# Performance work log

Measured on AMD Instinct MI355X. Metric: run time of the kernel, lower is better.

## Reference

```python
import jax, jax.numpy as jnp
import numpy as np

NEG_SLOPE = 0.2  # PyG GATConv default leaky_relu negative_slope
BN_EPS = 1e-5


def gat_layer(x, src, dst, W, a_src, a_dst, bias):
    """PyG-style GATConv (self-loops already appended to src/dst).
    x: [N, F_in], W: [F_in, H*C], a_src/a_dst: [H, C], bias: [H*C].
    Returns [N, H*C] (concat heads)."""
    N = x.shape[0]
    H, C = a_src.shape
    h = (x @ W).reshape(N, H, C)                      # [N, H, C]
    al_src = jnp.sum(h * a_src[None], axis=-1)        # [N, H]
    al_dst = jnp.sum(h * a_dst[None], axis=-1)        # [N, H]
    e = jax.nn.leaky_relu(al_src[src] + al_dst[dst], NEG_SLOPE)  # [E, H]
    # segment softmax over destination neighborhoods
    m = jax.ops.segment_max(e, dst, num_segments=N)   # [N, H]
    ee = jnp.exp(e - m[dst])
    denom = jax.ops.segment_sum(ee, dst, num_segments=N)  # [N, H]
    alpha = ee / denom[dst]                           # [E, H]
    out = jax.ops.segment_sum(alpha[:, :, None] * h[src], dst, num_segments=N)  # [N, H, C]
    return out.reshape(N, H * C) + bias


def batch_norm(x, gamma, beta):
    mu = jnp.mean(x, axis=0)
    var = jnp.var(x, axis=0)  # biased, matches torch BN training stats
    return gamma * (x - mu) * jax.lax.rsqrt(var + BN_EPS) + beta


def setup_inputs() -> dict:
    key = jax.random.key(0)
    N, F, H, C = 50000, 128, 4, 64
    E = 400000
    HC = H * C  # 256
    ks = jax.random.split(key, 24)

    def glorot(k, shape, fan_in):
        return jax.random.normal(k, shape, dtype=jnp.float32) * (1.0 / np.sqrt(fan_in))

    inp = {
        "x": jax.random.normal(ks[0], (N, F), dtype=jnp.float32),
        "edge_index": jax.random.randint(ks[1], (2, E), 0, N, dtype=jnp.int64),
        # conv1: F -> H*C
        "W1": glorot(ks[2], (F, HC), F),
        "a1s": glorot(ks[3], (H, C), C),
        "a1d": glorot(ks[4], (H, C), C),
        "b1": jnp.zeros((HC,), jnp.float32),
        # conv2: H*C -> H*C
        "W2": glorot(ks[5], (HC, HC), HC),
        "a2s": glorot(ks[6], (H, C), C),
        "a2d": glorot(ks[7], (H, C), C),
        "b2": jnp.zeros((HC,), jnp.float32),
        # conv3: H*C -> C (1 head)
        "W3": glorot(ks[8], (HC, C), HC),
        "a3s": glorot(ks[9], (1, C), C),
        "a3d": glorot(ks[10], (1, C), C),
        "b3": jnp.zeros((C,), jnp.float32),
        # batch norms
        "g1": jnp.ones((HC,), jnp.float32),
        "be1": jnp.zeros((HC,), jnp.float32),
        "g2": jnp.ones((HC,), jnp.float32),
        "be2": jnp.zeros((HC,), jnp.float32),
        # MLP head: C -> C//2 -> 2
        "fw1": glorot(ks[11], (C, C // 2), C),
        "fb1": jnp.zeros((C // 2,), jnp.float32),
        "fw2": glorot(ks[12], (C // 2, 2), C // 2),
        "fb2": jnp.zeros((2,), jnp.float32),
    }
    return inp


def reference(x, edge_index, W1, a1s, a1d, b1, W2, a2s, a2d, b2,
              W3, a3s, a3d, b3, g1, be1, g2, be2, fw1, fb1, fw2, fb2):
    N = x.shape[0]
    loop = jnp.arange(N, dtype=edge_index.dtype)
    src = jnp.concatenate([edge_index[0], loop])  # self-loops (PyG default)
    dst = jnp.concatenate([edge_index[1], loop])

    h = gat_layer(x, src, dst, W1, a1s, a1d, b1)
    h = jax.nn.elu(batch_norm(h, g1, be1))
    h = gat_layer(h, src, dst, W2, a2s, a2d, b2)
    h = jax.nn.elu(batch_norm(h, g2, be2))
    h = jax.nn.elu(gat_layer(h, src, dst, W3, a3s, a3d, b3))
    h = jax.nn.relu(h @ fw1 + fb1)
    return h @ fw2 + fb2  # [N, 2] logits
```

## Files before the change

### kernel.cpp

```cpp
#include <hip/hip_runtime.h>
#include <math.h>
#include <stdint.h>

typedef __attribute__((ext_vector_type(8))) short short8v;
typedef __attribute__((ext_vector_type(4))) float float4v;

__device__ __forceinline__ float bf2f(unsigned short u) {
  return __uint_as_float((unsigned int)u << 16);
}
__device__ __forceinline__ unsigned short f2bf(float f) {
  unsigned int u = __float_as_uint(f);
  unsigned int r = (u + 0x7FFFu + ((u >> 16) & 1u)) >> 16;
  return (unsigned short)r;
}
__device__ __forceinline__ float exp_lrelu(float x) {
  x = x > 0.f ? x : 0.2f * x;
  return expf(x);
}

__device__ __forceinline__ void wprep_one(const float* W, unsigned short* Wh,
                                          int t, int K, int Nw)
{
  int i = t & 7;
  int lane = (t >> 3) & 63;
  int frag = t >> 9;
  int ktiles = K >> 5;
  int n_tile = frag / ktiles, k_tile = frag - n_tile * ktiles;
  int k = k_tile * 32 + ((lane >> 4) << 3) + i;
  int n = (n_tile << 4) + (lane & 15);
  Wh[t] = f2bf(W[(size_t)k * Nw + n]);
}

__global__ void wprep_all_kernel(const float* __restrict__ W1, unsigned short* __restrict__ w1h,
                                 const float* __restrict__ W2, unsigned short* __restrict__ w2h,
                                 const float* __restrict__ W3, unsigned short* __restrict__ w3h)
{
  int t = blockIdx.x * 256 + threadIdx.x;
  const int s1 = 128 * 256, s2 = 256 * 256, s3 = 256 * 64;
  if (t < s1) { wprep_one(W1, w1h, t, 128, 256); return; }
  t -= s1;
  if (t < s2) { wprep_one(W2, w2h, t, 256, 256); return; }
  t -= s2;
  if (t < s3) { wprep_one(W3, w3h, t, 256, 64); }
}

template<int MI, int WM, int WN, int KSTEPS, int HEADS, bool SRCF32>
__global__ __launch_bounds__(128) void gemm_bn_al(
    const void* __restrict__ AsrcV,
    const float* __restrict__ scale, const float* __restrict__ shift,
    const unsigned short* __restrict__ Bh,
    const float* __restrict__ a_s, const float* __restrict__ a_d,
    unsigned short* __restrict__ C, float* __restrict__ al_s, float* __restrict__ al_d,
    int M)
{
  constexpr int BM = WM * MI * 16;
  constexpr int Nw = HEADS * 64;
  constexpr int K = KSTEPS * 64;
  constexpr int KT32 = KSTEPS * 2;
  __shared__ __align__(16) unsigned char smem[2][8192];

  const int tid = threadIdx.x;
  const int wid = tid >> 6, lane = tid & 63;
  const int wm = wid / WN, wn = wid % WN;
  const int gn = blockIdx.y * WN + wn;
  const int m0 = blockIdx.x * BM;
  const int n0 = gn * 64;
  const int ar = lane & 15;
  const int cchunk = lane >> 4;
  const int ntile0 = n0 >> 4;
  const int srow = min(m0 + (tid & 63), M - 1);

  float4v acc[MI][4];
#pragma unroll
  for (int mi = 0; mi < MI; ++mi)
#pragma unroll
    for (int ni = 0; ni < 4; ++ni)
      acc[mi][ni] = (float4v){0.f, 0.f, 0.f, 0.f};

  float4 rv0[4], rv1[4];
  short8v ru[4];

  auto LOADS = [&](int ks) {
#pragma unroll
    for (int j = 0; j < 4; ++j) {
      int c = 2 * j + wid;
      if constexpr (SRCF32) {
        const float* p = (const float*)AsrcV + (size_t)srow * K + ks * 64 + c * 8;
        rv0[j] = *(const float4*)p;
        rv1[j] = *(const float4*)(p + 4);
      } else {
        const unsigned short* p = (const unsigned short*)AsrcV + (size_t)srow * K + ks * 64 + c * 8;
        ru[j] = *(const short8v*)p;
      }
    }
  };
  auto XWRITE = [&](int buf, int ks) {
#pragma unroll
    for (int j = 0; j < 4; ++j) {
      int c = 2 * j + wid;
      int r = tid & 63;
      short8v wv;
      if constexpr (SRCF32) {
        float v[8] = {rv0[j].x, rv0[j].y, rv0[j].z, rv0[j].w,
                      rv1[j].x, rv1[j].y, rv1[j].z, rv1[j].w};
#pragma unroll
        for (int i = 0; i < 8; ++i) wv[i] = (short)f2bf(v[i]);
      } else {
        int f = ks * 64 + c * 8;
        float4 sc0 = *(const float4*)(scale + f), sc1 = *(const float4*)(scale + f + 4);
        float4 sh0 = *(const float4*)(shift + f), sh1 = *(const float4*)(shift + f + 4);
        float sc[8] = {sc0.x, sc0.y, sc0.z, sc0.w, sc1.x, sc1.y, sc1.z, sc1.w};
        float sh[8] = {sh0.x, sh0.y, sh0.z, sh0.w, sh1.x, sh1.y, sh1.z, sh1.w};
#pragma unroll
        for (int i = 0; i < 8; ++i) {
          float t = fmaf(bf2f((unsigned short)ru[j][i]), sc[i], sh[i]);
          t = t > 0.f ? t : expm1f(t);
          wv[i] = (short)f2bf(t);
        }
      }
      *(short8v*)&smem[buf][c * 1024 + r * 16] = wv;
    }
  };

  LOADS(0);
  XWRITE(0, 0);
  int cur = 0;
  for (int ks = 0; ks < KSTEPS; ++ks) {
    __syncthreads();
    short8v bh[2][4];
#pragma unroll
    for (int hh = 0; hh < 2; ++hh)
#pragma unroll
      for (int ni = 0; ni < 4; ++ni) {
        int kt = ks * 2 + hh;
        size_t off = (((size_t)(ntile0 + ni) * KT32 + kt) * 64 + lane) * 8;
        bh[hh][ni] = *(const short8v*)(Bh + off);
      }
    if (ks + 1 < KSTEPS) LOADS(ks + 1);
    short8v ah[2][MI];
#pragma unroll
    for (int hh = 0; hh < 2; ++hh)
#pragma unroll
      for (int mi = 0; mi < MI; ++mi) {
        int row = wm * MI * 16 + mi * 16 + ar;
        int c = hh * 4 + cchunk;
        ah[hh][mi] = *(const short8v*)&smem[cur][c * 1024 + row * 16];
      }
#pragma unroll
    for (int hh = 0; hh < 2; ++hh)
#pragma unroll
      for (int mi = 0; mi < MI; ++mi)
#pragma unroll
        for (int ni = 0; ni < 4; ++ni)
          acc[mi][ni] = __builtin_amdgcn_mfma_f32_16x16x32_bf16(ah[hh][mi], bh[hh][ni], acc[mi][ni], 0, 0, 0);
    if (ks + 1 < KSTEPS) XWRITE(cur ^ 1, ks + 1);
    cur ^= 1;
  }

  const int cc = lane & 15;
#pragma unroll
  for (int mi = 0; mi < MI; ++mi) {
    int rowb = m0 + wm * MI * 16 + mi * 16 + ((lane >> 4) << 2);
#pragma unroll
    for (int r = 0; r < 4; ++r) {
      int row = rowb + r;
      if (row < M) {
#pragma unroll
        for (int ni = 0; ni < 4; ++ni)
          C[(size_t)row * Nw + n0 + ni * 16 + cc] = f2bf(acc[mi][ni][r]);
      }
    }
  }

  const int head = (HEADS == 4) ? gn : 0;
  float as_[4], ad_[4];
#pragma unroll
  for (int ni = 0; ni < 4; ++ni) {
    as_[ni] = a_s[head * 64 + ni * 16 + cc];
    ad_[ni] = a_d[head * 64 + ni * 16 + cc];
  }
#pragma unroll
  for (int mi = 0; mi < MI; ++mi) {
#pragma unroll
    for (int r = 0; r < 4; ++r) {
      float h0 = bf2f(f2bf(acc[mi][0][r]));
      float h1 = bf2f(f2bf(acc[mi][1][r]));
      float h2 = bf2f(f2bf(acc[mi][2][r]));
      float h3 = bf2f(f2bf(acc[mi][3][r]));
      float ps = h0 * as_[0] + h1 * as_[1] + h2 * as_[2] + h3 * as_[3];
      float pd = h0 * ad_[0] + h1 * ad_[1] + h2 * ad_[2] + h3 * ad_[3];
#pragma unroll
      for (int off = 1; off < 16; off <<= 1) {
        ps += __shfl_xor(ps, off);
        pd += __shfl_xor(pd, off);
      }
      int row = m0 + wm * MI * 16 + mi * 16 + ((lane >> 4) << 2) + r;
      if (cc == 0 && row < M) {
        al_s[row * HEADS + head] = ps;
        al_d[row * HEADS + head] = pd;
      }
    }
  }
}

__global__ void count_kernel(const int* __restrict__ dst, int E, int Etot, int* __restrict__ counts)
{
  int e = blockIdx.x * 256 + threadIdx.x;
  if (e >= Etot) return;
  int d = (e < E) ? dst[e] : (e - E);
  atomicAdd(&counts[d], 1);
}

__global__ void block_sum_kernel(const int* __restrict__ counts, int N, int* __restrict__ bsums)
{
  __shared__ int sd[256];
  int i = blockIdx.x * 256 + threadIdx.x;
  sd[threadIdx.x] = (i < N) ? counts[i] : 0;
  __syncthreads();
  for (int off = 128; off; off >>= 1) {
    if (threadIdx.x < off) sd[threadIdx.x] += sd[threadIdx.x + off];
    __syncthreads();
  }
  if (threadIdx.x == 0) bsums[blockIdx.x] = sd[0];
}

__global__ void scan_bsums_kernel(int* bsums, int nb)
{
  __shared__ int sd[256];
  int t = threadIdx.x;
  int v = (t < nb) ? bsums[t] : 0;
  sd[t] = v;
  __syncthreads();
  for (int off = 1; off < 256; off <<= 1) {
    int x = (t >= off) ? sd[t - off] : 0;
    __syncthreads();
    sd[t] += x;
    __syncthreads();
  }
  if (t < nb) bsums[t] = sd[t] - v;
}

__global__ void scan_write_kernel(const int* __restrict__ counts, int N,
                                  const int* __restrict__ bsums, int* __restrict__ rowStart, int Etot)
{
  __shared__ int sd[256];
  int i = blockIdx.x * 256 + threadIdx.x;
  int v = (i < N) ? counts[i] : 0;
  sd[threadIdx.x] = v;
  __syncthreads();
  for (int off = 1; off < 256; off <<= 1) {
    int x = (threadIdx.x >= off) ? sd[threadIdx.x - off] : 0;
    __syncthreads();
    sd[threadIdx.x] += x;
    __syncthreads();
  }
  if (i < N) rowStart[i] = bsums[blockIdx.x] + sd[threadIdx.x] - v;
  if (i == N - 1) rowStart[N] = Etot;
}

__global__ void fill_kernel(const int* __restrict__ src, const int* __restrict__ dst,
                            int E, int Etot, const int* __restrict__ rowStart,
                            int* __restrict__ cursor, int* __restrict__ csrSrc)
{
  int e = blockIdx.x * 256 + threadIdx.x;
  if (e >= Etot) return;
  int s, d;
  if (e < E) { s = src[e]; d = dst[e]; } else { s = d = e - E; }
  int pos = rowStart[d] + atomicAdd(&cursor[d], 1);
  csrSrc[pos] = s;
}

__global__ __launch_bounds__(256) void aggregate_fused4(
    const unsigned short* __restrict__ h16,
    const float* __restrict__ als, const float* __restrict__ ald,
    const int* __restrict__ csrSrc, const int* __restrict__ rowStart,
    unsigned short* __restrict__ outp, int N)
{
  __shared__ float ldsW[4][256];
  const int wl = threadIdx.x >> 6;
  int wid = blockIdx.x * 4 + wl;
  if (wid >= N) return;
  const int lane = threadIdx.x & 63;
  const int head = lane >> 4;
  const int start = rowStart[wid], end = rowStart[wid + 1];

  float4 adv = ((const float4*)ald)[wid];
  float acc[4] = {};
  float wsum = 0.f;

  for (int base = start; base < end; base += 64) {
    int cnt = end - base; if (cnt > 64) cnt = 64;
    int s_l = 0;
    if (lane < cnt) {
      s_l = csrSrc[base + lane];
      float4 av = ((const float4*)als)[s_l];
      float4 w4;
      w4.x = exp_lrelu(av.x + adv.x);
      w4.y = exp_lrelu(av.y + adv.y);
      w4.z = exp_lrelu(av.z + adv.z);
      w4.w = exp_lrelu(av.w + adv.w);
      *(float4*)&ldsW[wl][lane * 4] = w4;
    }
    int i = 0;
    for (; i + 4 <= cnt; i += 4) {
      int s0 = __shfl(s_l, i);
      int s1 = __shfl(s_l, i + 1);
      int s2 = __shfl(s_l, i + 2);
      int s3 = __shfl(s_l, i + 3);
      float w0 = ldsW[wl][(i + 0) * 4 + head];
      float w1 = ldsW[wl][(i + 1) * 4 + head];
      float w2 = ldsW[wl][(i + 2) * 4 + head];
      float w3 = ldsW[wl][(i + 3) * 4 + head];
      ushort4 r0 = ((const ushort4*)(h16 + (size_t)s0 * 256))[lane];
      ushort4 r1 = ((const ushort4*)(h16 + (size_t)s1 * 256))[lane];
      ushort4 r2 = ((const ushort4*)(h16 + (size_t)s2 * 256))[lane];
      ushort4 r3 = ((const ushort4*)(h16 + (size_t)s3 * 256))[lane];
      wsum += (w0 + w1) + (w2 + w3);
      acc[0] = fmaf(w0, bf2f(r0.x), acc[0]);
      acc[1] = fmaf(w0, bf2f(r0.y), acc[1]);
      acc[2] = fmaf(w0, bf2f(r0.z), acc[2]);
      acc[3] = fmaf(w0, bf2f(r0.w), acc[3]);
      acc[0] = fmaf(w1, bf2f(r1.x), acc[0]);
      acc[1] = fmaf(w1, bf2f(r1.y), acc[1]);
      acc[2] = fmaf(w1, bf2f(r1.z), acc[2]);
      acc[3] = fmaf(w1, bf2f(r1.w), acc[3]);
      acc[0] = fmaf(w2, bf2f(r2.x), acc[0]);
      acc[1] = fmaf(w2, bf2f(r2.y), acc[1]);
      acc[2] = fmaf(w2, bf2f(r2.z), acc[2]);
      acc[3] = fmaf(w2, bf2f(r2.w), acc[3]);
      acc[0] = fmaf(w3, bf2f(r3.x), acc[0]);
      acc[1] = fmaf(w3, bf2f(r3.y), acc[1]);
      acc[2] = fmaf(w3, bf2f(r3.z), acc[2]);
      acc[3] = fmaf(w3, bf2f(r3.w), acc[3]);
    }
    for (; i < cnt; ++i) {
      int s0 = __shfl(s_l, i);
      float w0 = ldsW[wl][i * 4 + head];
      wsum += w0;
      ushort4 r0 = ((const ushort4*)(h16 + (size_t)s0 * 256))[lane];
      acc[0] = fmaf(w0, bf2f(r0.x), acc[0]);
      acc[1] = fmaf(w0, bf2f(r0.y), acc[1]);
      acc[2] = fmaf(w0, bf2f(r0.z), acc[2]);
      acc[3] = fmaf(w0, bf2f(r0.w), acc[3]);
    }
  }

  float inv = 1.0f / wsum;
  ushort4 o;
  o.x = f2bf(acc[0] * inv); o.y = f2bf(acc[1] * inv);
  o.z = f2bf(acc[2] * inv); o.w = f2bf(acc[3] * inv);
  ((ushort4*)(outp + (size_t)wid * 256))[lane] = o;
}

__global__ __launch_bounds__(256) void agg3_mlp_kernel(
    const unsigned short* __restrict__ h16,
    const float* __restrict__ als, const float* __restrict__ ald,
    const int* __restrict__ csrSrc, const int* __restrict__ rowStart,
    const float* __restrict__ b3,
    const float* __restrict__ fw1, const float* __restrict__ fb1,
    const float* __restrict__ fw2, const float* __restrict__ fb2,
    float* __restrict__ out, int N)
{
  __shared__ float ldsW[4][64];
  __shared__ float w1s[64][32];
  __shared__ float w2s[32][2];
  __shared__ float b1s[32];
  __shared__ float mrow[4][64];
  const int t = threadIdx.x;
  for (int i = t; i < 2048; i += 256) w1s[i >> 5][i & 31] = fw1[i];
  if (t < 64) w2s[t >> 1][t & 1] = fw2[t];
  if (t < 32) b1s[t] = fb1[t];
  __syncthreads();

  const int wl = t >> 6, lane = t & 63;
  int wid = blockIdx.x * 4 + wl;
  if (wid >= N) return;
  const int start = rowStart[wid], end = rowStart[wid + 1];
  const float ad0 = ald[wid];

  float acc = 0.f, wsum = 0.f;
  for (int base = start; base < end; base += 64) {
    int cnt = end - base; if (cnt > 64) cnt = 64;
    int s_l = 0;
    if (lane < cnt) {
      s_l = csrSrc[base + lane];
      ldsW[wl][lane] = exp_lrelu(als[s_l] + ad0);
    }
    int i = 0;
    for (; i + 4 <= cnt; i += 4) {
      int s0 = __shfl(s_l, i);
      int s1 = __shfl(s_l, i + 1);
      int s2 = __shfl(s_l, i + 2);
      int s3 = __shfl(s_l, i + 3);
      float w0 = ldsW[wl][i + 0];
      float w1 = ldsW[wl][i + 1];
      float w2 = ldsW[wl][i + 2];
      float w3 = ldsW[wl][i + 3];
      unsigned short r0 = h16[(size_t)s0 * 64 + lane];
      unsigned short r1 = h16[(size_t)s1 * 64 + lane];
      unsigned short r2 = h16[(size_t)s2 * 64 + lane];
      unsigned short r3 = h16[(size_t)s3 * 64 + lane];
      wsum += (w0 + w1) + (w2 + w3);
      acc = fmaf(w0, bf2f(r0), acc);
      acc = fmaf(w1, bf2f(r1), acc);
      acc = fmaf(w2, bf2f(r2), acc);
      acc = fmaf(w3, bf2f(r3), acc);
    }
    for (; i < cnt; ++i) {
      int s0 = __shfl(s_l, i);
      float w0 = ldsW[wl][i];
      wsum += w0;
      unsigned short r0 = h16[(size_t)s0 * 64 + lane];
      acc = fmaf(w0, bf2f(r0), acc);
    }
  }
  float o = acc / wsum + b3[lane];
  o = o > 0.f ? o : expm1f(o);

  mrow[wl][lane] = o;
  const int j = lane & 31, col = lane >> 5;
  float hid = b1s[j];
#pragma unroll
  for (int k = 0; k < 64; ++k)
    hid = fmaf(mrow[wl][k], w1s[k][j], hid);
  hid = fmaxf(hid, 0.f);
  float p = hid * w2s[j][col];
#pragma unroll
  for (int off = 1; off < 32; off <<= 1) p += __shfl_xor(p, off);
  if (j == 0) out[(size_t)wid * 2 + col] = p + fb2[col];
}

__global__ __launch_bounds__(256) void bn_stats_kernel(const unsigned short* __restrict__ x, int N,
                                float* __restrict__ partials)
{
  const int wid = threadIdx.x >> 6, lane = threadIdx.x & 63;
  const int gw = blockIdx.x * 4 + wid;
  const int tw = gridDim.x * 4;
  float4 s = make_float4(0.f, 0.f, 0.f, 0.f);
  float4 q = make_float4(0.f, 0.f, 0.f, 0.f);
#pragma unroll 4
  for (int r = gw; r < N; r += tw) {
    ushort4 u = ((const ushort4*)(x + (size_t)r * 256))[lane];
    float v0 = bf2f(u.x), v1 = bf2f(u.y), v2 = bf2f(u.z), v3 = bf2f(u.w);
    s.x += v0; s.y += v1; s.z += v2; s.w += v3;
    q.x = fmaf(v0, v0, q.x); q.y = fmaf(v1, v1, q.y);
    q.z = fmaf(v2, v2, q.z); q.w = fmaf(v3, v3, q.w);
  }
  __shared__ float ls[4][512];
  *(float4*)&ls[wid][lane * 4] = s;
  *(float4*)&ls[wid][256 + lane * 4] = q;
  __syncthreads();
  const int t = threadIdx.x;
  float a = ls[0][t] + ls[1][t] + ls[2][t] + ls[3][t];
  float b = ls[0][t + 256] + ls[1][t + 256] + ls[2][t + 256] + ls[3][t + 256];
  partials[blockIdx.x * 512 + t] = a;
  partials[blockIdx.x * 512 + 256 + t] = b;
}

__global__ void bn_final_kernel(const float* __restrict__ partials, int nblk,
                                const float* __restrict__ g, const float* __restrict__ be,
                                int N, float* __restrict__ scale, float* __restrict__ shift)
{
  int f = threadIdx.x;
  float s = 0.f, q = 0.f;
#pragma unroll 8
  for (int b = 0; b < nblk; ++b) {
    s += partials[b * 512 + f];
    q += partials[b * 512 + 256 + f];
  }
  float mu = s / N;
  float var = q / N - mu * mu;
  float rs = rsqrtf(var + 1e-5f);
  float sc = g[f] * rs;
  scale[f] = sc;
  shift[f] = be[f] - mu * sc;
}

extern "C" void kernel_launch(void* const* d_in, const int* in_sizes, int n_in,
                              void* d_out, int out_size, void* d_ws, size_t ws_size,
                              hipStream_t stream)
{
  const float* x   = (const float*)d_in[0];
  const int*   ei  = (const int*)d_in[1];
  const float* W1  = (const float*)d_in[2];
  const float* a1s = (const float*)d_in[3];
  const float* a1d = (const float*)d_in[4];
  const float* W2  = (const float*)d_in[6];
  const float* a2s = (const float*)d_in[7];
  const float* a2d = (const float*)d_in[8];
  const float* W3  = (const float*)d_in[10];
  const float* a3s = (const float*)d_in[11];
  const float* a3d = (const float*)d_in[12];
  const float* b3  = (const float*)d_in[13];
  const float* g1  = (const float*)d_in[14];
  const float* be1 = (const float*)d_in[15];
  const float* g2  = (const float*)d_in[16];
  const float* be2 = (const float*)d_in[17];
  const float* fw1 = (const float*)d_in[18];
  const float* fb1 = (const float*)d_in[19];
  const float* fw2 = (const float*)d_in[20];
  const float* fb2 = (const float*)d_in[21];
  float* out = (float*)d_out;

  const int F = 128;
  const int N = in_sizes[0] / F;
  const int E = in_sizes[1] / 2;
  const int Etot = E + N;
  const int* srcIdx = ei;
  const int* dstIdx = ei + E;

  char* w = (char*)d_ws;
  auto alloc = [&](size_t bytes) -> void* {
    void* p = (void*)w;
    w += (bytes + 255) & ~(size_t)255;
    return p;
  };
  unsigned short* h16  = (unsigned short*)alloc((size_t)N * 256 * 2);
  unsigned short* act16= (unsigned short*)alloc((size_t)N * 256 * 2);
  float* als     = (float*)alloc((size_t)N * 4 * 4);
  float* ald     = (float*)alloc((size_t)N * 4 * 4);
  const size_t cntPad = ((size_t)N * 4 + 255) & ~(size_t)255;
  int*   counts  = (int*)alloc((size_t)N * 4);
  int*   cursor  = (int*)alloc((size_t)N * 4);
  int*   rowStart= (int*)alloc((size_t)(N + 1) * 4);
  int*   csrSrc  = (int*)alloc((size_t)Etot * 4);
  int*   bsums   = (int*)alloc((size_t)((N + 255) / 256) * 4);
  float* partials= (float*)alloc((size_t)128 * 512 * 4);
  float* scale1  = (float*)alloc(256 * 4);
  float* shift1  = (float*)alloc(256 * 4);
  float* scale2  = (float*)alloc(256 * 4);
  float* shift2  = (float*)alloc(256 * 4);
  unsigned short* w1h = (unsigned short*)alloc((size_t)128 * 256 * 2);
  unsigned short* w2h = (unsigned short*)alloc((size_t)256 * 256 * 2);
  unsigned short* w3h = (unsigned short*)alloc((size_t)256 * 64 * 2);
  (void)alloc(65536);

  const int nb = (N + 255) / 256;
  const int ebk = (Etot + 255) / 256;
  const int aggBlocks = (N + 3) / 4;

  const int wtot = 128 * 256 + 256 * 256 + 256 * 64;
  wprep_all_kernel<<<(wtot + 255) / 256, 256, 0, stream>>>(W1, w1h, W2, w2h, W3, w3h);

  hipMemsetAsync(counts, 0, cntPad + (size_t)N * 4, stream);
  count_kernel<<<ebk, 256, 0, stream>>>(dstIdx, E, Etot, counts);
  block_sum_kernel<<<nb, 256, 0, stream>>>(counts, N, bsums);
  scan_bsums_kernel<<<1, 256, 0, stream>>>(bsums, nb);
  scan_write_kernel<<<nb, 256, 0, stream>>>(counts, N, bsums, rowStart, Etot);
  fill_kernel<<<ebk, 256, 0, stream>>>(srcIdx, dstIdx, E, Etot, rowStart, cursor, csrSrc);

  dim3 g12((N + 63) / 64, 2);
  dim3 g3((N + 63) / 64, 1);

  gemm_bn_al<4, 1, 2, 2, 4, true><<<g12, 128, 0, stream>>>(
      x, nullptr, nullptr, w1h, a1s, a1d, h16, als, ald, N);
  aggregate_fused4<<<aggBlocks, 256, 0, stream>>>(h16, als, ald, csrSrc, rowStart, act16, N);
  bn_stats_kernel<<<128, 256, 0, stream>>>(act16, N, partials);
  bn_final_kernel<<<1, 256, 0, stream>>>(partials, 128, g1, be1, N, scale1, shift1);

  gemm_bn_al<4, 1, 2, 4, 4, false><<<g12, 128, 0, stream>>>(
      act16, scale1, shift1, w2h, a2s, a2d, h16, als, ald, N);
  aggregate_fused4<<<aggBlocks, 256, 0, stream>>>(h16, als, ald, csrSrc, rowStart, act16, N);
  bn_stats_kernel<<<128, 256, 0, stream>>>(act16, N, partials);
  bn_final_kernel<<<1, 256, 0, stream>>>(partials, 128, g2, be2, N, scale2, shift2);

  gemm_bn_al<2, 2, 1, 4, 1, false><<<g3, 128, 0, stream>>>(
      act16, scale2, shift2, w3h, a3s, a3d, h16, als, ald, N);
  agg3_mlp_kernel<<<aggBlocks, 256, 0, stream>>>(h16, als, ald, csrSrc, rowStart,
                                                 b3, fw1, fb1, fw2, fb2, out, N);
}
```

Before: 314.9 us.

## Split BN/convert out of GEMM, use direct global-to-LDS loads, fuse BN finalize

```diff
diff --git a/kernel.cpp b/kernel.cpp
--- a/kernel.cpp
+++ b/kernel.cpp
@@ -16,6 +16,12 @@
 __device__ __forceinline__ float exp_lrelu(float x) {
   x = x > 0.f ? x : 0.2f * x;
   return expf(x);
+}
+
+typedef __attribute__((address_space(3))) void lds_void;
+typedef const __attribute__((address_space(1))) void glb_void;
+__device__ __forceinline__ void gload_lds16(const void* g, void* l) {
+  __builtin_amdgcn_global_load_lds((glb_void*)g, (lds_void*)l, 16, 0, 0);
 }
 
 __device__ __forceinline__ void wprep_one(const float* W, unsigned short* Wh,
@@ -44,23 +50,60 @@
   if (t < s3) { wprep_one(W3, w3h, t, 256, 64); }
 }
 
-template<int MI, int WM, int WN, int KSTEPS, int HEADS, bool SRCF32>
-__global__ __launch_bounds__(128) void gemm_bn_al(
-    const void* __restrict__ AsrcV,
+__global__ __launch_bounds__(256) void split_kernel(const float* __restrict__ in,
+    unsigned short* __restrict__ hi, size_t n4)
+{
+  size_t i0 = (size_t)blockIdx.x * 256 + threadIdx.x;
+  size_t stride = (size_t)gridDim.x * 256;
+  for (size_t idx = i0; idx < n4; idx += stride) {
+    float4 v = ((const float4*)in)[idx];
+    ushort4 h;
+    h.x = f2bf(v.x); h.y = f2bf(v.y); h.z = f2bf(v.z); h.w = f2bf(v.w);
+    ((ushort4*)hi)[idx] = h;
+  }
+}
+
+__global__ __launch_bounds__(256) void bnsplit_kernel(const unsigned short* __restrict__ act,
     const float* __restrict__ scale, const float* __restrict__ shift,
-    const unsigned short* __restrict__ Bh,
+    unsigned short* __restrict__ hi, size_t nchunks)
+{
+  size_t i0 = (size_t)blockIdx.x * 256 + threadIdx.x;
+  size_t stride = (size_t)gridDim.x * 256;
+  for (size_t idx = i0; idx < nchunks; idx += stride) {
+    ushort4 u = ((const ushort4*)act)[idx];
+    int f = (int)((idx * 4) & 255);
+    float4 sc = *(const float4*)(scale + f);
+    float4 sh = *(const float4*)(shift + f);
+    float v0 = fmaf(bf2f(u.x), sc.x, sh.x);
+    float v1 = fmaf(bf2f(u.y), sc.y, sh.y);
+    float v2 = fmaf(bf2f(u.z), sc.z, sh.z);
+    float v3 = fmaf(bf2f(u.w), sc.w, sh.w);
+    v0 = v0 > 0.f ? v0 : expm1f(v0);
+    v1 = v1 > 0.f ? v1 : expm1f(v1);
+    v2 = v2 > 0.f ? v2 : expm1f(v2);
+    v3 = v3 > 0.f ? v3 : expm1f(v3);
+    ushort4 h;
+    h.x = f2bf(v0); h.y = f2bf(v1); h.z = f2bf(v2); h.w = f2bf(v3);
+    ((ushort4*)hi)[idx] = h;
+  }
+}
+
+template<int MI, int WM, int WN, int KSTEPS, int HEADS>
+__global__ __launch_bounds__(128) void gemm_al(
+    const unsigned short* __restrict__ Ah, const unsigned short* __restrict__ Bh,
     const float* __restrict__ a_s, const float* __restrict__ a_d,
     unsigned short* __restrict__ C, float* __restrict__ al_s, float* __restrict__ al_d,
     int M)
 {
+  constexpr int NWAVES = WM * WN;
   constexpr int BM = WM * MI * 16;
+  constexpr int TILEB = BM * 64 * 2;
   constexpr int Nw = HEADS * 64;
   constexpr int K = KSTEPS * 64;
   constexpr int KT32 = KSTEPS * 2;
-  __shared__ __align__(16) unsigned char smem[2][8192];
-
-  const int tid = threadIdx.x;
-  const int wid = tid >> 6, lane = tid & 63;
+  __shared__ __align__(16) unsigned char smem[2][TILEB];
+
+  const int wid = threadIdx.x >> 6, lane = threadIdx.x & 63;
   const int wm = wid / WN, wn = wid % WN;
   const int gn = blockIdx.y * WN + wn;
   const int m0 = blockIdx.x * BM;
@@ -68,7 +111,6 @@
   const int ar = lane & 15;
   const int cchunk = lane >> 4;
   const int ntile0 = n0 >> 4;
-  const int srow = min(m0 + (tid & 63), M - 1);
 
   float4v acc[MI][4];
 #pragma unroll
@@ -77,53 +119,15 @@
     for (int ni = 0; ni < 4; ++ni)
       acc[mi][ni] = (float4v){0.f, 0.f, 0.f, 0.f};
 
-  float4 rv0[4], rv1[4];
-  short8v ru[4];
-
-  auto LOADS = [&](int ks) {
-#pragma unroll
-    for (int j = 0; j < 4; ++j) {
-      int c = 2 * j + wid;
-      if constexpr (SRCF32) {
-        const float* p = (const float*)AsrcV + (size_t)srow * K + ks * 64 + c * 8;
-        rv0[j] = *(const float4*)p;
-        rv1[j] = *(const float4*)(p + 4);
-      } else {
-        const unsigned short* p = (const unsigned short*)AsrcV + (size_t)srow * K + ks * 64 + c * 8;
-        ru[j] = *(const short8v*)p;
-      }
+  auto stage = [&](int buf, int ks) {
+#pragma unroll
+    for (int c = wid; c < 8; c += NWAVES) {
+      const unsigned short* gp = Ah + (size_t)(m0 + lane) * K + ks * 64 + c * 8;
+      gload_lds16(gp, &smem[buf][c * 1024 + lane * 16]);
     }
   };
-  auto XWRITE = [&](int buf, int ks) {
-#pragma unroll
-    for (int j = 0; j < 4; ++j) {
-      int c = 2 * j + wid;
-      int r = tid & 63;
-      short8v wv;
-      if constexpr (SRCF32) {
-        float v[8] = {rv0[j].x, rv0[j].y, rv0[j].z, rv0[j].w,
-                      rv1[j].x, rv1[j].y, rv1[j].z, rv1[j].w};
-#pragma unroll
-        for (int i = 0; i < 8; ++i) wv[i] = (short)f2bf(v[i]);
-      } else {
-        int f = ks * 64 + c * 8;
-        float4 sc0 = *(const float4*)(scale + f), sc1 = *(const float4*)(scale + f + 4);
-        float4 sh0 = *(const float4*)(shift + f), sh1 = *(const float4*)(shift + f + 4);
-        float sc[8] = {sc0.x, sc0.y, sc0.z, sc0.w, sc1.x, sc1.y, sc1.z, sc1.w};
-        float sh[8] = {sh0.x, sh0.y, sh0.z, sh0.w, sh1.x, sh1.y, sh1.z, sh1.w};
-#pragma unroll
-        for (int i = 0; i < 8; ++i) {
-          float t = fmaf(bf2f((unsigned short)ru[j][i]), sc[i], sh[i]);
-          t = t > 0.f ? t : expm1f(t);
-          wv[i] = (short)f2bf(t);
-        }
-      }
-      *(short8v*)&smem[buf][c * 1024 + r * 16] = wv;
-    }
-  };
-
-  LOADS(0);
-  XWRITE(0, 0);
+
+  stage(0, 0);
   int cur = 0;
   for (int ks = 0; ks < KSTEPS; ++ks) {
     __syncthreads();
@@ -136,7 +140,7 @@
         size_t off = (((size_t)(ntile0 + ni) * KT32 + kt) * 64 + lane) * 8;
         bh[hh][ni] = *(const short8v*)(Bh + off);
       }
-    if (ks + 1 < KSTEPS) LOADS(ks + 1);
+    if (ks + 1 < KSTEPS) stage(cur ^ 1, ks + 1);
     short8v ah[2][MI];
 #pragma unroll
     for (int hh = 0; hh < 2; ++hh)
@@ -153,7 +157,6 @@
 #pragma unroll
         for (int ni = 0; ni < 4; ++ni)
           acc[mi][ni] = __builtin_amdgcn_mfma_f32_16x16x32_bf16(ah[hh][mi], bh[hh][ni], acc[mi][ni], 0, 0, 0);
-    if (ks + 1 < KSTEPS) XWRITE(cur ^ 1, ks + 1);
     cur ^= 1;
   }
 
@@ -203,9 +206,11 @@
   }
 }
 
-__global__ void count_kernel(const int* __restrict__ dst, int E, int Etot, int* __restrict__ counts)
+__global__ void count_kernel(const int* __restrict__ dst, int E, int Etot,
+                             int* __restrict__ counts, unsigned int* __restrict__ bnCounter)
 {
   int e = blockIdx.x * 256 + threadIdx.x;
+  if (blockIdx.x == 0 && threadIdx.x == 0) *bnCounter = 0;
   if (e >= Etot) return;
   int d = (e < E) ? dst[e] : (e - E);
   atomicAdd(&counts[d], 1);
@@ -430,8 +435,11 @@
   if (j == 0) out[(size_t)wid * 2 + col] = p + fb2[col];
 }
 
-__global__ __launch_bounds__(256) void bn_stats_kernel(const unsigned short* __restrict__ x, int N,
-                                float* __restrict__ partials)
+__global__ __launch_bounds__(256) void bn_stats_final_kernel(
+    const unsigned short* __restrict__ x, int N,
+    float* __restrict__ partials, unsigned int* __restrict__ counter,
+    const float* __restrict__ g, const float* __restrict__ be,
+    float* __restrict__ scale, float* __restrict__ shift)
 {
   const int wid = threadIdx.x >> 6, lane = threadIdx.x & 63;
   const int gw = blockIdx.x * 4 + wid;
@@ -455,25 +463,28 @@
   float b = ls[0][t + 256] + ls[1][t + 256] + ls[2][t + 256] + ls[3][t + 256];
   partials[blockIdx.x * 512 + t] = a;
   partials[blockIdx.x * 512 + 256 + t] = b;
-}
-
-__global__ void bn_final_kernel(const float* __restrict__ partials, int nblk,
-                                const float* __restrict__ g, const float* __restrict__ be,
-                                int N, float* __restrict__ scale, float* __restrict__ shift)
-{
-  int f = threadIdx.x;
-  float s = 0.f, q = 0.f;
-#pragma unroll 8
-  for (int b = 0; b < nblk; ++b) {
-    s += partials[b * 512 + f];
-    q += partials[b * 512 + 256 + f];
-  }
-  float mu = s / N;
-  float var = q / N - mu * mu;
-  float rs = rsqrtf(var + 1e-5f);
-  float sc = g[f] * rs;
-  scale[f] = sc;
-  shift[f] = be[f] - mu * sc;
+
+  __threadfence();
+  __shared__ unsigned int done;
+  if (t == 0) done = atomicAdd(counter, 1u);
+  __syncthreads();
+  if (done == gridDim.x - 1) {
+    __threadfence();
+    const volatile float* vp = partials;
+    float ss = 0.f, qq = 0.f;
+    const int nblk = gridDim.x;
+    for (int bb = 0; bb < nblk; ++bb) {
+      ss += vp[bb * 512 + t];
+      qq += vp[bb * 512 + 256 + t];
+    }
+    float mu = ss / N;
+    float var = qq / N - mu * mu;
+    float rs = rsqrtf(var + 1e-5f);
+    float sc = g[t] * rs;
+    scale[t] = sc;
+    shift[t] = be[t] - mu * sc;
+    if (t == 0) *counter = 0;
+  }
 }
 
 extern "C" void kernel_launch(void* const* d_in, const int* in_sizes, int n_in,
@@ -517,6 +528,7 @@
   };
   unsigned short* h16  = (unsigned short*)alloc((size_t)N * 256 * 2);
   unsigned short* act16= (unsigned short*)alloc((size_t)N * 256 * 2);
+  unsigned short* aBf  = (unsigned short*)alloc((size_t)N * 256 * 2);
   float* als     = (float*)alloc((size_t)N * 4 * 4);
   float* ald     = (float*)alloc((size_t)N * 4 * 4);
   const size_t cntPad = ((size_t)N * 4 + 255) & ~(size_t)255;
@@ -526,6 +538,7 @@
   int*   csrSrc  = (int*)alloc((size_t)Etot * 4);
   int*   bsums   = (int*)alloc((size_t)((N + 255) / 256) * 4);
   float* partials= (float*)alloc((size_t)128 * 512 * 4);
+  unsigned int* bnCounter = (unsigned int*)alloc(256);
   float* scale1  = (float*)alloc(256 * 4);
   float* shift1  = (float*)alloc(256 * 4);
   float* scale2  = (float*)alloc(256 * 4);
@@ -543,7 +556,7 @@
   wprep_all_kernel<<<(wtot + 255) / 256, 256, 0, stream>>>(W1, w1h, W2, w2h, W3, w3h);
 
   hipMemsetAsync(counts, 0, cntPad + (size_t)N * 4, stream);
-  count_kernel<<<ebk, 256, 0, stream>>>(dstIdx, E, Etot, counts);
+  count_kernel<<<ebk, 256, 0, stream>>>(dstIdx, E, Etot, counts, bnCounter);
   block_sum_kernel<<<nb, 256, 0, stream>>>(counts, N, bsums);
   scan_bsums_kernel<<<1, 256, 0, stream>>>(bsums, nb);
   scan_write_kernel<<<nb, 256, 0, stream>>>(counts, N, bsums, rowStart, Etot);
@@ -552,20 +565,18 @@
   dim3 g12((N + 63) / 64, 2);
   dim3 g3((N + 63) / 64, 1);
 
-  gemm_bn_al<4, 1, 2, 2, 4, true><<<g12, 128, 0, stream>>>(
-      x, nullptr, nullptr, w1h, a1s, a1d, h16, als, ald, N);
+  split_kernel<<<2048, 256, 0, stream>>>(x, aBf, (size_t)N * 128 / 4);
+  gemm_al<4, 1, 2, 2, 4><<<g12, 128, 0, stream>>>(aBf, w1h, a1s, a1d, h16, als, ald, N);
   aggregate_fused4<<<aggBlocks, 256, 0, stream>>>(h16, als, ald, csrSrc, rowStart, act16, N);
-  bn_stats_kernel<<<128, 256, 0, stream>>>(act16, N, partials);
-  bn_final_kernel<<<1, 256, 0, stream>>>(partials, 128, g1, be1, N, scale1, shift1);
-
-  gemm_bn_al<4, 1, 2, 4, 4, false><<<g12, 128, 0, stream>>>(
-      act16, scale1, shift1, w2h, a2s, a2d, h16, als, ald, N);
+  bn_stats_final_kernel<<<128, 256, 0, stream>>>(act16, N, partials, bnCounter, g1, be1, scale1, shift1);
+
+  bnsplit_kernel<<<2048, 256, 0, stream>>>(act16, scale1, shift1, aBf, (size_t)N * 64);
+  gemm_al<4, 1, 2, 4, 4><<<g12, 128, 0, stream>>>(aBf, w2h, a2s, a2d, h16, als, ald, N);
   aggregate_fused4<<<aggBlocks, 256, 0, stream>>>(h16, als, ald, csrSrc, rowStart, act16, N);
-  bn_stats_kernel<<<128, 256, 0, stream>>>(act16, N, partials);
-  bn_final_kernel<<<1, 256, 0, stream>>>(partials, 128, g2, be2, N, scale2, shift2);
-
-  gemm_bn_al<2, 2, 1, 4, 1, false><<<g3, 128, 0, stream>>>(
-      act16, scale2, shift2, w3h, a3s, a3d, h16, als, ald, N);
+  bn_stats_final_kernel<<<128, 256, 0, stream>>>(act16, N, partials, bnCounter, g2, be2, scale2, shift2);
+
+  bnsplit_kernel<<<2048, 256, 0, stream>>>(act16, scale2, shift2, aBf, (size_t)N * 64);
+  gemm_al<2, 2, 1, 4, 1><<<g3, 128, 0, stream>>>(aBf, w3h, a3s, a3d, h16, als, ald, N);
   agg3_mlp_kernel<<<aggBlocks, 256, 0, stream>>>(h16, als, ald, csrSrc, rowStart,
                                                  b3, fw1, fb1, fw2, fb2, out, N);
 }
```

Measured after the change: 431.0 us. +36.9%, slower.
